# Kernel tuning notes

Hardware: AMD Instinct MI355X
Metric: run time of the kernel (lower is better)

Reference implementation:

```python
import jax, jax.numpy as jnp
import numpy as np

B, N = 128, 2048
DX = 10.0 / 2048.0   # X / N
DT = 5.0e-4          # CFL-consistent timestep


def f_real(u):
    # f(u) = 0.5*u*(3 - u^2) + (300/12)*u^2*(3/4 - 2u + 3/2 u^2 - 1/4 u^4)
    u2 = u * u
    return 0.5 * u * (3.0 - u2) + 25.0 * u2 * (0.75 - 2.0 * u + 1.5 * u2 - 0.25 * u2 * u2)


def dfdu_abs(u):
    # f_real is elementwise, so grad of the sum gives the elementwise derivative,
    # matching torch.autograd.grad(f, u, grad_outputs=ones_like(f))
    return jnp.abs(jax.grad(lambda uu: jnp.sum(f_real(uu)))(u))


def setup_inputs() -> dict:
    key = jax.random.key(0)
    init = jax.random.uniform(key, (B, N), dtype=jnp.float32)  # u in [0,1]
    return {"init": init, "stepnum": 500}


def reference(init, stepnum):
    lam = jnp.float32(DT / DX)

    def step(u_old, _):
        f = f_real(u_old)                      # [B, N]
        a = dfdu_abs(u_old)                    # |f'(u)|, [B, N]
        # local Lax-Friedrichs flux: max over the (j, j+1) pair
        alpha = jnp.maximum(a[:, :-1], a[:, 1:])  # [B, N-1]
        f_half = 0.5 * (f[:, :-1] + f[:, 1:]) - 0.5 * alpha * (u_old[:, 1:] - u_old[:, :-1])
        interior = u_old[:, 1:-1] - lam * (f_half[:, 1:] - f_half[:, :-1])  # [B, N-2]
        # boundary: u[:,0]=u[:,1], u[:,N-1]=u[:,N-2]
        u = jnp.concatenate([interior[:, :1], interior, interior[:, -1:]], axis=1)
        return u, u

    _, traj = jax.lax.scan(step, init, None, length=stepnum - 1)  # [stepnum-1, B, N]
    return jnp.concatenate([init[None], traj], axis=0)            # [stepnum, B, N]
```

## Files before the change

### kernel.cpp

```cpp
#include <hip/hip_runtime.h>

#define NPTS 2048
#define TPB  768
#define CAP  1536

typedef float v2f __attribute__((ext_vector_type(2)));

#define EDGE_BARRIER() do {                                   \
    asm volatile("s_waitcnt lgkmcnt(0)" ::: "memory");        \
    __builtin_amdgcn_s_barrier();                             \
    asm volatile("" ::: "memory");                            \
} while (0)

__device__ __forceinline__ v2f s2(float x) { v2f v; v.x = x; v.y = x; return v; }

__device__ __forceinline__ v2f fma2(v2f a, v2f b, v2f c) {
#if __has_builtin(__builtin_elementwise_fma)
    return __builtin_elementwise_fma(a, b, c);
#else
    v2f r; r.x = fmaf(a.x, b.x, c.x); r.y = fmaf(a.y, b.y, c.y); return r;
#endif
}

__device__ __forceinline__ void eval_gq2(v2f u, v2f& g, v2f& q) {
    const v2f uu = u * u;
    v2f gg = fma2(uu, s2(-3.125f), s2(18.75f));
    gg = fma2(u, gg, s2(-25.25f));
    gg = fma2(u, gg, s2(9.375f));
    gg = fma2(u, gg, s2(0.75f));
    g = u * gg;
    v2f pp = fma2(uu, s2(-37.5f), s2(150.0f));
    pp = fma2(u, pp, s2(-151.5f));
    pp = fma2(u, pp, s2(37.5f));
    v2f p = fma2(u, pp, s2(1.5f));
    v2f ap; ap.x = fabsf(p.x); ap.y = fabsf(p.y);
    q = ap * s2(0.5f);
}

__global__ __launch_bounds__(TPB) void lxf_split(
    const float* __restrict__ init, float* __restrict__ out,
    int nbatch, int nsteps)
{
    __shared__ float Ub[2][CAP];
    __shared__ float Gb[2][CAP];
    __shared__ float Qb[2][CAP];

    const int blk = blockIdx.x;
    const int r   = blk >> 1;
    const int h   = blk & 1;
    const int tid = threadIdx.x;
    const int c0  = 2 * tid;
    const int gb  = h ? 512 : 0;
    const size_t rowoff = (size_t)r * NPTS;
    const float lam = 0.1024f;

    const bool st  = h ? (c0 >= 512) : (c0 < 1024);
    const bool bcL = (h == 0) && (tid == 0);
    const bool bcR = (h == 1) && (tid == TPB - 1);
    const int dist = h ? (509 - c0) : (c0 - 1025);

    v2f uv = *reinterpret_cast<const v2f*>(init + rowoff + gb + c0);
    v2f gv, qv;
    eval_gq2(uv, gv, qv);

    if (st) *reinterpret_cast<v2f*>(out + rowoff + gb + c0) = uv;

    *reinterpret_cast<v2f*>(&Ub[0][c0]) = uv;
    *reinterpret_cast<v2f*>(&Gb[0][c0]) = gv;
    *reinterpret_cast<v2f*>(&Qb[0][c0]) = qv;
    EDGE_BARRIER();

    const size_t stride = (size_t)nbatch * NPTS;
    float* dstw = out + rowoff + gb + c0;

#define STEP(CUR, NXT) do {                                              \
    dstw += stride;                                                      \
    if (dist <= rem) {                                                   \
        const float* bu = &Ub[CUR][0] + (c0 - 1);                        \
        const float* bg = &Gb[CUR][0] + (c0 - 1);                        \
        const float* bq = &Qb[CUR][0] + (c0 - 1);                        \
        float uL = bu[0], uR = bu[3];                                    \
        float gL = bg[0], gR = bg[3];                                    \
        float qL = bq[0], qR = bq[3];                                    \
        if (tid == 0)       { uL = uv.x; gL = gv.x; qL = qv.x; }         \
        if (tid == TPB - 1) { uR = uv.y; gR = gv.y; qR = qv.y; }         \
        const float aL = fmaxf(qL, qv.x);                                \
        const float aM = fmaxf(qv.x, qv.y);                              \
        const float aR = fmaxf(qv.y, qR);                                \
        const float fhL = fmaf(-aL, uv.x - uL, gL + gv.x);               \
        const float fhM = fmaf(-aM, uv.y - uv.x, gv.x + gv.y);           \
        const float fhR = fmaf(-aR, uR - uv.y, gv.y + gR);               \
        float n0 = fmaf(-lam, fhM - fhL, uv.x);                          \
        float n1 = fmaf(-lam, fhR - fhM, uv.y);                          \
        if (bcL) n0 = n1;                           \
        if (bcR) n1 = n0;                           \
        uv.x = n0; uv.y = n1;                                            \
        eval_gq2(uv, gv, qv);                                            \
        *reinterpret_cast<v2f*>(&Ub[NXT][c0]) = uv;                      \
        *reinterpret_cast<v2f*>(&Gb[NXT][c0]) = gv;                      \
        *reinterpret_cast<v2f*>(&Qb[NXT][c0]) = qv;                      \
        if (st) *reinterpret_cast<v2f*>(dstw) = uv;                      \
    }                                                                    \
    --rem;                                                               \
    EDGE_BARRIER();                                                      \
} while (0)

    const int S  = nsteps - 1;
    int rem = S - 1;
    const int P2 = S >> 1;
    for (int i = 0; i < P2; ++i) {
        STEP(0, 1);
        STEP(1, 0);
    }
    if (S & 1) STEP(0, 1);
#undef STEP
}

extern "C" void kernel_launch(void* const* d_in, const int* in_sizes, int n_in,
                              void* d_out, int out_size, void* d_ws, size_t ws_size,
                              hipStream_t stream) {
    const float* init = (const float*)d_in[0];
    float* out = (float*)d_out;

    const int nbatch = in_sizes[0] / NPTS;
    const int nsteps = out_size / in_sizes[0];

    hipLaunchKernelGGL(lxf_split, dim3(2 * nbatch), dim3(TPB), 0, stream,
                       init, out, nbatch, nsteps);
}
```

Measured before the change: 171.4 us.

## Split time integration into chunked launches with smaller overlapping halo windows

Replaces the single launch, which integrates all steps per half-row with a 1536-point window, with several launches that each advance 125 steps. Each launch restarts from the state stored in the output buffer, so the redundant halo shrinks to 128 points and the window to 1152 points with 576 threads. Neighbour indices are now precomputed and clamped, removing the per-step boundary branches. In exchange it adds four kernel launches and a global reload of the state at each chunk boundary.

```diff
diff --git a/kernel.cpp b/kernel.cpp
--- a/kernel.cpp
+++ b/kernel.cpp
@@ -1,8 +1,9 @@
 #include <hip/hip_runtime.h>
 
-#define NPTS 2048
-#define TPB  768
-#define CAP  1536
+#define NPTS   2048
+#define TPB    576
+#define WIN    1152
+#define TCHUNK 125
 
 typedef float v2f __attribute__((ext_vector_type(2)));
 
@@ -37,53 +38,50 @@
     q = ap * s2(0.5f);
 }
 
-__global__ __launch_bounds__(TPB) void lxf_split(
-    const float* __restrict__ init, float* __restrict__ out,
-    int nbatch, int nsteps)
+__global__ __launch_bounds__(TPB) void lxf_tc(
+    const float* __restrict__ srcrow, float* __restrict__ out,
+    int nbatch, int t0, int nsub, int copy0)
 {
-    __shared__ float Ub[2][CAP];
-    __shared__ float Gb[2][CAP];
-    __shared__ float Qb[2][CAP];
+    __shared__ float Ub[2][WIN];
+    __shared__ float Gb[2][WIN];
+    __shared__ float Qb[2][WIN];
 
     const int blk = blockIdx.x;
     const int r   = blk >> 1;
     const int h   = blk & 1;
     const int tid = threadIdx.x;
     const int c0  = 2 * tid;
-    const int gb  = h ? 512 : 0;
-    const size_t rowoff = (size_t)r * NPTS;
+    const int wb  = h ? (NPTS - WIN) : 0;
     const float lam = 0.1024f;
 
-    const bool st  = h ? (c0 >= 512) : (c0 < 1024);
+    const bool st  = h ? (c0 >= 128) : (c0 < 1024);
     const bool bcL = (h == 0) && (tid == 0);
     const bool bcR = (h == 1) && (tid == TPB - 1);
-    const int dist = h ? (509 - c0) : (c0 - 1025);
+    const int  hl  = (tid == 0)       ? 0       : c0 - 1;
+    const int  hr  = (tid == TPB - 1) ? WIN - 1 : c0 + 2;
+    const int dist = h ? (125 - c0) : (c0 - 1025);
 
-    v2f uv = *reinterpret_cast<const v2f*>(init + rowoff + gb + c0);
+    v2f uv = *reinterpret_cast<const v2f*>(srcrow + (size_t)r * NPTS + wb + c0);
     v2f gv, qv;
     eval_gq2(uv, gv, qv);
 
-    if (st) *reinterpret_cast<v2f*>(out + rowoff + gb + c0) = uv;
+    const size_t stride = (size_t)nbatch * NPTS;
+    float* sp = out + (size_t)t0 * stride + (size_t)r * NPTS + (wb + c0);
+    if (copy0 && st) *reinterpret_cast<v2f*>(sp) = uv;
 
     *reinterpret_cast<v2f*>(&Ub[0][c0]) = uv;
     *reinterpret_cast<v2f*>(&Gb[0][c0]) = gv;
     *reinterpret_cast<v2f*>(&Qb[0][c0]) = qv;
     EDGE_BARRIER();
 
-    const size_t stride = (size_t)nbatch * NPTS;
-    float* dstw = out + rowoff + gb + c0;
+    float* dstw = sp;
+    int rem = nsub - 1;
 
 #define STEP(CUR, NXT) do {                                              \
     dstw += stride;                                                      \
     if (dist <= rem) {                                                   \
-        const float* bu = &Ub[CUR][0] + (c0 - 1);                        \
-        const float* bg = &Gb[CUR][0] + (c0 - 1);                        \
-        const float* bq = &Qb[CUR][0] + (c0 - 1);                        \
-        float uL = bu[0], uR = bu[3];                                    \
-        float gL = bg[0], gR = bg[3];                                    \
-        float qL = bq[0], qR = bq[3];                                    \
-        if (tid == 0)       { uL = uv.x; gL = gv.x; qL = qv.x; }         \
-        if (tid == TPB - 1) { uR = uv.y; gR = gv.y; qR = qv.y; }         \
+        const float uL = Ub[CUR][hl], gL = Gb[CUR][hl], qL = Qb[CUR][hl];\
+        const float uR = Ub[CUR][hr], gR = Gb[CUR][hr], qR = Qb[CUR][hr];\
         const float aL = fmaxf(qL, qv.x);                                \
         const float aM = fmaxf(qv.x, qv.y);                              \
         const float aR = fmaxf(qv.y, qR);                                \
@@ -105,14 +103,12 @@
     EDGE_BARRIER();                                                      \
 } while (0)
 
-    const int S  = nsteps - 1;
-    int rem = S - 1;
-    const int P2 = S >> 1;
+    const int P2 = nsub >> 1;
     for (int i = 0; i < P2; ++i) {
         STEP(0, 1);
         STEP(1, 0);
     }
-    if (S & 1) STEP(0, 1);
+    if (nsub & 1) STEP(0, 1);
 #undef STEP
 }
 
@@ -124,7 +120,18 @@
 
     const int nbatch = in_sizes[0] / NPTS;
     const int nsteps = out_size / in_sizes[0];
+    const int S = nsteps - 1;
+    const size_t stride = (size_t)nbatch * NPTS;
 
-    hipLaunchKernelGGL(lxf_split, dim3(2 * nbatch), dim3(TPB), 0, stream,
-                       init, out, nbatch, nsteps);
+    int t0 = 0;
+    int first = 1;
+    while (t0 < S) {
+        int nsub = S - t0;
+        if (nsub > TCHUNK) nsub = TCHUNK;
+        const float* srcrow = first ? init : (out + (size_t)t0 * stride);
+        hipLaunchKernelGGL(lxf_tc, dim3(2 * nbatch), dim3(TPB), 0, stream,
+                           srcrow, out, nbatch, t0, nsub, first);
+        t0 += nsub;
+        first = 0;
+    }
 }
```

Measured after the change: 170.8 us. No clear change (-0.3%).
